# Optimization experiments

Measured on AMD Instinct MI355X. Metric: run time of the kernel, lower is better.

Reference implementation:

```python
import jax, jax.numpy as jnp
import numpy as np

B, IN, COND, H, LAT, E, GH = 8192, 256, 1024, 1024, 128, 6, 64
INP = LAT + COND      # decoder layer0 input size = 1152
INTER = LAT + H       # decoder layer1/2 input size = 1152


def setup_inputs() -> dict:
    key = jax.random.key(0)
    ks = jax.random.split(key, 30)
    n = lambda k, shape, s=0.02: jax.random.normal(k, shape, dtype=jnp.float32) * s
    return {
        'x': jax.random.normal(ks[0], (B, IN), dtype=jnp.float32),
        'y': jax.random.normal(ks[1], (B, COND), dtype=jnp.float32),
        'eps': jax.random.normal(ks[2], (B, LAT), dtype=jnp.float32),
        # encoder: layer k input = prev_dim + IN (x is re-concatenated each layer)
        'enc_w0': n(ks[3], (IN + COND + IN, H)), 'enc_b0': jnp.zeros((H,), jnp.float32),
        'enc_w1': n(ks[4], (H + IN, H)),         'enc_b1': jnp.zeros((H,), jnp.float32),
        'mu_w': n(ks[5], (H, LAT)),  'mu_b': jnp.zeros((LAT,), jnp.float32),
        'lv_w': n(ks[6], (H, LAT)),  'lv_b': jnp.zeros((LAT,), jnp.float32),
        # gating network (input = latent + cond)
        'g_w0': n(ks[7], (INP, GH)), 'g_b0': jnp.zeros((GH,), jnp.float32),
        'g_w1': n(ks[8], (GH, GH)),  'g_b1': jnp.zeros((GH,), jnp.float32),
        'g_w2': n(ks[9], (GH, E)),   'g_b2': jnp.zeros((E,), jnp.float32),
        # expert weights [E, in, out] and biases [E, out] (bias init 0.01 as in source)
        'exp_w0': n(ks[10], (E, INP, H)),   'exp_b0': jnp.full((E, H), 0.01, jnp.float32),
        'exp_w1': n(ks[11], (E, INTER, H)), 'exp_b1': jnp.full((E, H), 0.01, jnp.float32),
        'exp_w2': n(ks[12], (E, INTER, IN)), 'exp_b2': jnp.full((E, IN), 0.01, jnp.float32),
    }


def _forward(x, y, eps, enc_w0, enc_b0, enc_w1, enc_b1, mu_w, mu_b, lv_w, lv_b,
             g_w0, g_b0, g_w1, g_b1, g_w2, g_b2,
             exp_w0, exp_b0, exp_w1, exp_b1, exp_w2, exp_b2):
    elu = jax.nn.elu
    # --- Encoder ---
    h = jnp.concatenate([x, y], axis=1)
    h = elu(jnp.concatenate([h, x], axis=1) @ enc_w0 + enc_b0)
    h = elu(jnp.concatenate([h, x], axis=1) @ enc_w1 + enc_b1)
    mu = h @ mu_w + mu_b
    logvar = h @ lv_w + lv_b
    # --- Reparameterize (eps passed explicitly for determinism) ---
    z = mu + eps * jnp.exp(0.5 * logvar)
    # --- MixedDecoder ---
    g = jnp.concatenate([z, y], axis=1)
    g = elu(g @ g_w0 + g_b0)
    g = elu(g @ g_w1 + g_b1)
    coeff = jax.nn.softmax(g @ g_w2 + g_b2, axis=1)  # [B, E]
    layer_out = y
    for W, bb, act in ((exp_w0, exp_b0, True), (exp_w1, exp_b1, True), (exp_w2, exp_b2, False)):
        inp = jnp.concatenate([z, layer_out], axis=1)  # [B, I]
        # fused mixture-of-experts projection: avoids materializing per-sample [B,I,O] weight
        out = coeff @ bb + jnp.einsum('be,bi,eio->bo', coeff, inp, W)
        layer_out = elu(out) if act else out
    return layer_out, mu, logvar


def reference(x, y, eps, enc_w0, enc_b0, enc_w1, enc_b1, mu_w, mu_b, lv_w, lv_b,
              g_w0, g_b0, g_w1, g_b1, g_w2, g_b2,
              exp_w0, exp_b0, exp_w1, exp_b1, exp_w2, exp_b2):
    return _forward(x, y, eps, enc_w0, enc_b0, enc_w1, enc_b1, mu_w, mu_b, lv_w, lv_b,
                    g_w0, g_b0, g_w1, g_b1, g_w2, g_b2,
                    exp_w0, exp_b0, exp_w1, exp_b1, exp_w2, exp_b2)
```

## Files before the change

kernel.cpp:

```cpp
#include <hip/hip_runtime.h>
#include <hip/hip_bf16.h>
#include <cstddef>

using u16 = unsigned short;
using short8 = __attribute__((ext_vector_type(8))) short;
using f32x4 = __attribute__((ext_vector_type(4))) float;

constexpr int B_   = 8192;
constexpr int IN_  = 256;
constexpr int COND_= 1024;
constexpr int H_   = 1024;
constexpr int LAT_ = 128;
constexpr int NE_  = 6;
constexpr int GH_  = 64;
constexpr int INP_ = 1152;
constexpr int K0_  = 1536;
constexpr int K1_  = 1280;

constexpr int BK = 64;

typedef const __attribute__((address_space(1))) void gv_t;
typedef __attribute__((address_space(3))) void lv_t;
#define GLDS(g, l) __builtin_amdgcn_global_load_lds((gv_t*)(g), (lv_t*)(l), 16, 0, 0)

__device__ __forceinline__ u16 f2b(float f) {
  __hip_bfloat16 h = __float2bfloat16(f);
  return *reinterpret_cast<u16*>(&h);
}
__device__ __forceinline__ ushort4 f2b4(float4 v) {
  ushort4 o;
  o.x = f2b(v.x); o.y = f2b(v.y); o.z = f2b(v.z); o.w = f2b(v.w);
  return o;
}
__device__ __forceinline__ float elu1(float x) { return x > 0.f ? x : (__expf(x) - 1.f); }

__global__ void k_transpose(const float* __restrict__ in, u16* __restrict__ out,
                            int R, int C, long inStride, long outStride) {
  __shared__ float t[32][33];
  const float* ip = in + (long)blockIdx.z * inStride;
  u16* op = out + (long)blockIdx.z * outStride;
  int c0 = blockIdx.x * 32, r0 = blockIdx.y * 32;
  int tx = threadIdx.x, ty = threadIdx.y;
#pragma unroll
  for (int i = 0; i < 4; i++) {
    int r = r0 + ty + i * 8, c = c0 + tx;
    if (r < R && c < C) t[ty + i * 8][tx] = ip[(long)r * C + c];
  }
  __syncthreads();
#pragma unroll
  for (int i = 0; i < 4; i++) {
    int c = c0 + ty + i * 8, r = r0 + tx;
    if (r < R && c < C) op[(long)c * R + r] = f2b(t[tx][ty + i * 8]);
  }
}

__global__ __launch_bounds__(256) void k_pre(
    const float* __restrict__ enc_w0, const float* __restrict__ enc_w1,
    const float* __restrict__ mu_w, const float* __restrict__ lv_w,
    const float* __restrict__ g_w0, const float* __restrict__ exp_w0,
    const float* __restrict__ x, const float* __restrict__ y,
    u16* __restrict__ encw0T, u16* __restrict__ encw1T, u16* __restrict__ mulvT,
    u16* __restrict__ gw0T, u16* __restrict__ ew0T,
    u16* __restrict__ A0, u16* __restrict__ A1)
{
  __shared__ float t[32][33];
  const int b = blockIdx.x;
  const int tid = threadIdx.x;
  const int tx = tid & 31, ty = tid >> 5;

  auto tr = [&](const float* in, u16* out, int R, int C, int bx, int by) {
    int c0 = bx * 32, r0 = by * 32;
#pragma unroll
    for (int i = 0; i < 4; i++) {
      int r = r0 + ty + i * 8, c = c0 + tx;
      if (r < R && c < C) t[ty + i * 8][tx] = in[(long)r * C + c];
    }
    __syncthreads();
#pragma unroll
    for (int i = 0; i < 4; i++) {
      int c = c0 + ty + i * 8, r = r0 + tx;
      if (r < R && c < C) out[(long)c * R + r] = f2b(t[tx][ty + i * 8]);
    }
  };

  if (b < 1536)       { tr(enc_w0, encw0T, K0_, H_, b & 31, b >> 5); }
  else if (b < 2816)  { int l = b - 1536; tr(enc_w1, encw1T, K1_, H_, l & 31, l >> 5); }
  else if (b < 2944)  { int l = b - 2816; tr(mu_w, mulvT, H_, LAT_, l & 3, l >> 2); }
  else if (b < 3072)  { int l = b - 2944; tr(lv_w, mulvT + (size_t)LAT_ * H_, H_, LAT_, l & 3, l >> 2); }
  else if (b < 3144)  { int l = b - 3072; tr(g_w0, gw0T, INP_, GH_, l & 1, l >> 1); }
  else if (b < 10056) {
    int l = b - 3144, e = l / 1152, r2 = l % 1152;
    tr(exp_w0 + (long)e * INP_ * H_, ew0T + (long)e * INP_ * H_, INP_, H_, r2 & 31, r2 >> 5);
  } else {
    long idx = (long)(b - 10056) * 256 + tid;
    long n0v = (long)B_ * K0_ / 4;
    if (idx < n0v) {
      long base = idx * 4;
      int bb = (int)(base / K0_), c = (int)(base % K0_);
      float4 v;
      if (c < IN_)              v = *(const float4*)&x[(long)bb * IN_ + c];
      else if (c < IN_ + COND_) v = *(const float4*)&y[(long)bb * COND_ + (c - IN_)];
      else                      v = *(const float4*)&x[(long)bb * IN_ + (c - IN_ - COND_)];
      *(ushort4*)&A0[base] = f2b4(v);
    } else {
      long j = idx - n0v;
      if (j < (long)B_ * IN_ / 4) {
        long base = j * 4;
        int bb = (int)(base / IN_), c = (int)(base % IN_);
        float4 v = *(const float4*)&x[(long)bb * IN_ + c];
        *(ushort4*)&A1[(long)bb * K1_ + H_ + c] = f2b4(v);
      }
    }
  }
}

__global__ __launch_bounds__(256) void k_mid(
    const float* __restrict__ exp_w2, u16* __restrict__ ew2T,
    const float* __restrict__ mu, const float* __restrict__ lv,
    const float* __restrict__ eps, const float* __restrict__ y,
    u16* __restrict__ ZY, u16* __restrict__ D1, u16* __restrict__ D2)
{
  __shared__ float t[32][33];
  const int b = blockIdx.x;
  const int tid = threadIdx.x;
  if (b < 1728) {
    const int tx = tid & 31, ty = tid >> 5;
    int e = b / 288, r2 = b % 288;
    const float* in = exp_w2 + (long)e * INP_ * IN_;
    u16* out = ew2T + (long)e * INP_ * IN_;
    int c0 = (r2 & 7) * 32, r0 = (r2 >> 3) * 32;
#pragma unroll
    for (int i = 0; i < 4; i++) {
      int r = r0 + ty + i * 8, c = c0 + tx;
      if (r < INP_ && c < IN_) t[ty + i * 8][tx] = in[(long)r * IN_ + c];
    }
    __syncthreads();
#pragma unroll
    for (int i = 0; i < 4; i++) {
      int c = c0 + ty + i * 8, r = r0 + tx;
      if (r < INP_ && c < IN_) out[(long)c * INP_ + r] = f2b(t[tx][ty + i * 8]);
    }
  } else {
    long idx = (long)(b - 1728) * 256 + tid;
    if (idx >= (long)B_ * INP_ / 4) return;
    long base = idx * 4;
    int bb = (int)(base / INP_), c = (int)(base % INP_);
    if (c < LAT_) {
      long o = (long)bb * LAT_ + c;
      float4 m = *(const float4*)&mu[o];
      float4 l = *(const float4*)&lv[o];
      float4 e4 = *(const float4*)&eps[o];
      float4 z;
      z.x = m.x + e4.x * __expf(0.5f * l.x);
      z.y = m.y + e4.y * __expf(0.5f * l.y);
      z.z = m.z + e4.z * __expf(0.5f * l.z);
      z.w = m.w + e4.w * __expf(0.5f * l.w);
      ushort4 zb = f2b4(z);
      *(ushort4*)&ZY[base] = zb;
      *(ushort4*)&D1[base] = zb;
      *(ushort4*)&D2[base] = zb;
    } else {
      float4 v = *(const float4*)&y[(long)bb * COND_ + (c - LAT_)];
      *(ushort4*)&ZY[base] = f2b4(v);
    }
  }
}

__global__ __launch_bounds__(256) void k_gate(const float* __restrict__ G1,
    const float* __restrict__ w1, const float* __restrict__ b1,
    const float* __restrict__ w2, const float* __restrict__ b2,
    float* __restrict__ coeff) {
  __shared__ float W1[64][65];
  __shared__ float W2[64][8];
  __shared__ float B1[64], B2[8];
  int tid = threadIdx.x;
  for (int i = tid; i < 64 * 64; i += 256) W1[i >> 6][i & 63] = w1[i];
  for (int i = tid; i < 64 * 6; i += 256) W2[i / 6][i % 6] = w2[i];
  if (tid < 64) B1[tid] = b1[tid];
  if (tid < 8)  B2[tid] = (tid < 6) ? b2[tid] : 0.f;
  __syncthreads();
  int row = blockIdx.x * 256 + tid;
  const float* gr = G1 + (long)row * GH_;
  float g[64];
#pragma unroll
  for (int i = 0; i < 16; i++) {
    float4 v = *(const float4*)(gr + i * 4);
    g[i*4] = v.x; g[i*4+1] = v.y; g[i*4+2] = v.z; g[i*4+3] = v.w;
  }
  float lg[6];
#pragma unroll
  for (int e = 0; e < 6; e++) lg[e] = B2[e];
  for (int n = 0; n < 64; n++) {
    float s = B1[n];
#pragma unroll
    for (int k = 0; k < 64; k++) s += g[k] * W1[k][n];
    s = elu1(s);
#pragma unroll
    for (int e = 0; e < 6; e++) lg[e] += s * W2[n][e];
  }
  float m = lg[0];
#pragma unroll
  for (int e = 1; e < 6; e++) m = fmaxf(m, lg[e]);
  float p[6], sum = 0.f;
#pragma unroll
  for (int e = 0; e < 6; e++) { p[e] = __expf(lg[e] - m); sum += p[e]; }
  float inv = 1.f / sum;
#pragma unroll
  for (int e = 0; e < 6; e++) coeff[(long)row * 6 + e] = p[e] * inv;
}

template<int KSTEPS, int E, bool MOE>
__global__ __launch_bounds__(512, 2) void k_gemm8(
    const u16* __restrict__ A,
    const u16* __restrict__ WT,
    const float* __restrict__ bias,
    const float* __restrict__ coeff,
    int N,
    u16* __restrict__ outH, int ldo)
{
  constexpr int KK = KSTEPS * BK;
  constexpr int T = E * KSTEPS;
  __shared__ __align__(16) u16 As[3][256][BK];
  __shared__ __align__(16) u16 Bs[3][128][BK];
  __shared__ float Cf[MOE ? 256 : 1][8];

  const int tid = threadIdx.x;
  const int lane = tid & 63, w = tid >> 6;
  const int wr = w >> 1, wc = w & 1;
  const int lin = blockIdx.x + blockIdx.y * gridDim.x;
  const int rb  = (lin & 7) * 4 + ((lin >> 3) & 3);
  const int cp  = lin >> 5;
  const int brow = rb * 256, bcol = cp * 128;
  const int lr = lane & 15, hi = lane >> 4;
  const int lk = hi * 8;
  const int xsw = (lr & 7) << 3;

  if (MOE) {
    if (tid < 256) {
#pragma unroll
      for (int e2 = 0; e2 < 8; e2++)
        Cf[tid][e2] = (e2 < 6) ? coeff[(long)(brow + tid) * 6 + e2] : 0.f;
    }
    __syncthreads();
  }

  f32x4 acc[4][4];
#pragma unroll
  for (int m = 0; m < 4; m++)
#pragma unroll
    for (int n = 0; n < 4; n++)
#pragma unroll
      for (int r = 0; r < 4; r++) acc[m][n][r] = 0.f;
  f32x4 pacc[MOE ? 4 : 1][MOE ? 4 : 1];
  if constexpr (MOE) {
#pragma unroll
    for (int m = 0; m < 4; m++)
#pragma unroll
      for (int n = 0; n < 4; n++)
#pragma unroll
        for (int r = 0; r < 4; r++) pacc[m][n][r] = 0.f;
  }

  const int srow = w * 8 + (lane >> 3);
  const int sdst = (lane & 7) * 8;
  const int ssrc = ((lane & 7) ^ ((lane >> 3) & 7)) * 8;
  const u16* Asrc = A + (long)(brow + srow) * KK + ssrc;
  const u16* Bsrc = WT + (long)(bcol + srow) * KK + ssrc;

  auto STAGE_H = [&](int t2, int buf, int h) {
    const int e2 = (E == 1) ? 0 : (t2 / KSTEPS);
    int k2 = (E == 1) ? t2 : (t2 % KSTEPS);
    if (E > 1 && (e2 & 1)) k2 = KSTEPS - 1 - k2;
    const u16* ap = Asrc + (long)k2 * BK;
    const u16* bp = Bsrc + (long)e2 * ((long)N * KK) + (long)k2 * BK;
    GLDS(ap + (long)((h * 2 + 0) * 64) * KK, &As[buf][(h * 2 + 0) * 64 + srow][sdst]);
    GLDS(ap + (long)((h * 2 + 1) * 64) * KK, &As[buf][(h * 2 + 1) * 64 + srow][sdst]);
    GLDS(bp + (long)(h * 64) * KK,           &Bs[buf][h * 64 + srow][sdst]);
  };

  STAGE_H(0, 0, 0); STAGE_H(0, 0, 1);
  STAGE_H(1, 1, 0); STAGE_H(1, 1, 1);
  asm volatile("s_waitcnt vmcnt(6)" ::: "memory");
  asm volatile("s_barrier" ::: "memory");

  for (int t = 0; t < T; ++t) {
    const int cur = t % 3;
    const int nbuf = (t + 2) % 3;
    const bool do_stage = (t + 2 < T);

    {
      short8 af[4], bfr[4];
      const int cc = lk ^ xsw;
#pragma unroll
      for (int m = 0; m < 4; m++)
        af[m] = *(const short8*)&As[cur][wr * 64 + m * 16 + lr][cc];
#pragma unroll
      for (int n = 0; n < 4; n++)
        bfr[n] = *(const short8*)&Bs[cur][wc * 64 + n * 16 + lr][cc];
      if (do_stage) STAGE_H(t + 2, nbuf, 0);
      asm volatile("s_barrier" ::: "memory");
      __builtin_amdgcn_s_setprio(1);
#pragma unroll
      for (int m = 0; m < 4; m++)
#pragma unroll
        for (int n = 0; n < 4; n++) {
          if constexpr (MOE)
            pacc[m][n] = __builtin_amdgcn_mfma_f32_16x16x32_bf16(af[m], bfr[n], pacc[m][n], 0, 0, 0);
          else
            acc[m][n] = __builtin_amdgcn_mfma_f32_16x16x32_bf16(af[m], bfr[n], acc[m][n], 0, 0, 0);
        }
      __builtin_amdgcn_s_setprio(0);
      asm volatile("s_barrier" ::: "memory");
    }

    {
      short8 af[4], bfr[4];
      const int cc = (32 + lk) ^ xsw;
#pragma unroll
      for (int m = 0; m < 4; m++)
        af[m] = *(const short8*)&As[cur][wr * 64 + m * 16 + lr][cc];
#pragma unroll
      for (int n = 0; n < 4; n++)
        bfr[n] = *(const short8*)&Bs[cur][wc * 64 + n * 16 + lr][cc];
      if (do_stage) STAGE_H(t + 2, nbuf, 1);
      asm volatile("s_barrier" ::: "memory");
      __builtin_amdgcn_s_setprio(1);
#pragma unroll
      for (int m = 0; m < 4; m++)
#pragma unroll
        for (int n = 0; n < 4; n++) {
          if constexpr (MOE)
            pacc[m][n] = __builtin_amdgcn_mfma_f32_16x16x32_bf16(af[m], bfr[n], pacc[m][n], 0, 0, 0);
          else
            acc[m][n] = __builtin_amdgcn_mfma_f32_16x16x32_bf16(af[m], bfr[n], acc[m][n], 0, 0, 0);
        }
      __builtin_amdgcn_s_setprio(0);
      if (t + 1 < T) {
        if (do_stage) asm volatile("s_waitcnt vmcnt(6)" ::: "memory");
        else          asm volatile("s_waitcnt vmcnt(0)" ::: "memory");
      }
      asm volatile("s_barrier" ::: "memory");
    }

    if constexpr (MOE) {
      if ((t + 1) % KSTEPS == 0) {
        const int e = t / KSTEPS;
#pragma unroll
        for (int m = 0; m < 4; m++)
#pragma unroll
          for (int r = 0; r < 4; r++) {
            float c = Cf[wr * 64 + m * 16 + hi * 4 + r][e];
#pragma unroll
            for (int n = 0; n < 4; n++) acc[m][n][r] += c * pacc[m][n][r];
          }
        if (t + 1 < T) {
#pragma unroll
          for (int m = 0; m < 4; m++)
#pragma unroll
            for (int n = 0; n < 4; n++)
#pragma unroll
              for (int r = 0; r < 4; r++) pacc[m][n][r] = 0.f;
        }
      }
    }
  }

#pragma unroll
  for (int m = 0; m < 4; m++)
#pragma unroll
    for (int n = 0; n < 4; n++) {
      const int col = bcol + wc * 64 + n * 16 + lr;
#pragma unroll
      for (int r = 0; r < 4; r++) {
        const int rowl = wr * 64 + m * 16 + hi * 4 + r;
        const long row = brow + rowl;
        float v = acc[m][n][r];
        if constexpr (MOE) {
          float bv = 0.f;
#pragma unroll
          for (int e = 0; e < 6; e++) bv += Cf[rowl][e] * bias[(long)e * N + col];
          v += bv;
        } else {
          v += bias[col];
        }
        v = elu1(v);
        outH[row * (long)ldo + col] = f2b(v);
      }
    }
}

template<int KSTEPS, int E, bool MOE>
__global__ __launch_bounds__(256, 2) void k_m2(
    const u16* __restrict__ A,
    const u16* __restrict__ WT,
    const float* __restrict__ bias, const float* __restrict__ bias2,
    const float* __restrict__ coeff,
    int N,
    u16* __restrict__ outH, float* __restrict__ outF, float* __restrict__ outF2,
    int ldo, int splitcol, int act)
{
  constexpr int KK = KSTEPS * BK;
  constexpr int T = E * KSTEPS;
  __shared__ __align__(16) u16 As[3][64][BK];
  __shared__ __align__(16) u16 Bs[3][128][BK];
  __shared__ float Cf[MOE ? 64 : 1][8];

  const int tid = threadIdx.x;
  const int lane = tid & 63, w = tid >> 6;
  const int wr = w >> 1, wc = w & 1;
  const int brow = blockIdx.x * 64, bcol = blockIdx.y * 128;
  const int lr = lane & 15, hi = lane >> 4;
  const int lk = hi * 8;
  const int xsw = (lr & 7) << 3;

  if (MOE) {
    if (tid < 64) {
#pragma unroll
      for (int e2 = 0; e2 < 8; e2++)
        Cf[tid][e2] = (e2 < 6) ? coeff[(long)(brow + tid) * 6 + e2] : 0.f;
    }
    __syncthreads();
  }

  f32x4 acc[2][4];
#pragma unroll
  for (int m = 0; m < 2; m++)
#pragma unroll
    for (int n = 0; n < 4; n++)
#pragma unroll
      for (int r = 0; r < 4; r++) acc[m][n][r] = 0.f;
  f32x4 pacc[MOE ? 2 : 1][MOE ? 4 : 1];
  if constexpr (MOE) {
#pragma unroll
    for (int m = 0; m < 2; m++)
#pragma unroll
      for (int n = 0; n < 4; n++)
#pragma unroll
        for (int r = 0; r < 4; r++) pacc[m][n][r] = 0.f;
  }

  const int srow = w * 8 + (lane >> 3);
  const int sdst = (lane & 7) * 8;
  const int ssrc = ((lane & 7) ^ ((lane >> 3) & 7)) * 8;
  const u16* Asrc = A + (long)(brow + srow) * KK + ssrc;
  const u16* Bsrc = WT + (long)(bcol + srow) * KK + ssrc;

  auto STAGE_H = [&](int t2, int buf, int h) {
    const int e2 = (E == 1) ? 0 : (t2 / KSTEPS);
    int k2 = (E == 1) ? t2 : (t2 % KSTEPS);
    if (E > 1 && (e2 & 1)) k2 = KSTEPS - 1 - k2;
    const u16* ap = Asrc + (long)k2 * BK;
    const u16* bp = Bsrc + (long)e2 * ((long)N * KK) + (long)k2 * BK;
    GLDS(ap + (long)(h * 32) * KK,            &As[buf][h * 32 + srow][sdst]);
    GLDS(bp + (long)(h * 64) * KK,            &Bs[buf][h * 64 + srow][sdst]);
    GLDS(bp + (long)(h * 64 + 32) * KK,       &Bs[buf][h * 64 + 32 + srow][sdst]);
  };

  STAGE_H(0, 0, 0); STAGE_H(0, 0, 1);
  STAGE_H(1, 1, 0); STAGE_H(1, 1, 1);
  asm volatile("s_waitcnt vmcnt(6)" ::: "memory");
  asm volatile("s_barrier" ::: "memory");

  for (int t = 0; t < T; ++t) {
    const int cur = t % 3;
    const int nbuf = (t + 2) % 3;
    const bool do_stage = (t + 2 < T);

    {
      short8 af[2], bfr[4];
      const int cc = lk ^ xsw;
#pragma unroll
      for (int m = 0; m < 2; m++)
        af[m] = *(const short8*)&As[cur][wr * 32 + m * 16 + lr][cc];
#pragma unroll
      for (int n = 0; n < 4; n++)
        bfr[n] = *(const short8*)&Bs[cur][wc * 64 + n * 16 + lr][cc];
      if (do_stage) STAGE_H(t + 2, nbuf, 0);
      asm volatile("s_barrier" ::: "memory");
      __builtin_amdgcn_s_setprio(1);
#pragma unroll
      for (int m = 0; m < 2; m++)
#pragma unroll
        for (int n = 0; n < 4; n++) {
          if constexpr (MOE)
            pacc[m][n] = __builtin_amdgcn_mfma_f32_16x16x32_bf16(af[m], bfr[n], pacc[m][n], 0, 0, 0);
          else
            acc[m][n] = __builtin_amdgcn_mfma_f32_16x16x32_bf16(af[m], bfr[n], acc[m][n], 0, 0, 0);
        }
      __builtin_amdgcn_s_setprio(0);
      asm volatile("s_barrier" ::: "memory");
    }
    {
      short8 af[2], bfr[4];
      const int cc = (32 + lk) ^ xsw;
#pragma unroll
      for (int m = 0; m < 2; m++)
        af[m] = *(const short8*)&As[cur][wr * 32 + m * 16 + lr][cc];
#pragma unroll
      for (int n = 0; n < 4; n++)
        bfr[n] = *(const short8*)&Bs[cur][wc * 64 + n * 16 + lr][cc];
      if (do_stage) STAGE_H(t + 2, nbuf, 1);
      asm volatile("s_barrier" ::: "memory");
      __builtin_amdgcn_s_setprio(1);
#pragma unroll
      for (int m = 0; m < 2; m++)
#pragma unroll
        for (int n = 0; n < 4; n++) {
          if constexpr (MOE)
            pacc[m][n] = __builtin_amdgcn_mfma_f32_16x16x32_bf16(af[m], bfr[n], pacc[m][n], 0, 0, 0);
          else
            acc[m][n] = __builtin_amdgcn_mfma_f32_16x16x32_bf16(af[m], bfr[n], acc[m][n], 0, 0, 0);
        }
      __builtin_amdgcn_s_setprio(0);
      if (t + 1 < T) {
        if (do_stage) asm volatile("s_waitcnt vmcnt(6)" ::: "memory");
        else          asm volatile("s_waitcnt vmcnt(0)" ::: "memory");
      }
      asm volatile("s_barrier" ::: "memory");
    }

    if constexpr (MOE) {
      if ((t + 1) % KSTEPS == 0) {
        const int e = t / KSTEPS;
#pragma unroll
        for (int m = 0; m < 2; m++)
#pragma unroll
          for (int r = 0; r < 4; r++) {
            float c = Cf[wr * 32 + m * 16 + hi * 4 + r][e];
#pragma unroll
            for (int n = 0; n < 4; n++) acc[m][n][r] += c * pacc[m][n][r];
          }
        if (t + 1 < T) {
#pragma unroll
          for (int m = 0; m < 2; m++)
#pragma unroll
            for (int n = 0; n < 4; n++)
#pragma unroll
              for (int r = 0; r < 4; r++) pacc[m][n][r] = 0.f;
        }
      }
    }
  }

#pragma unroll
  for (int m = 0; m < 2; m++)
#pragma unroll
    for (int n = 0; n < 4; n++) {
      const int col = bcol + wc * 64 + n * 16 + lr;
      if (col >= N) continue;
#pragma unroll
      for (int r = 0; r < 4; r++) {
        const int rowl = wr * 32 + m * 16 + hi * 4 + r;
        const long row = brow + rowl;
        float v = acc[m][n][r];
        if constexpr (MOE) {
          float bv = 0.f;
#pragma unroll
          for (int e = 0; e < 6; e++) bv += Cf[rowl][e] * bias[(long)e * N + col];
          v += bv;
        } else {
          v += (col < splitcol) ? bias[col] : bias2[col - splitcol];
        }
        if (act) v = elu1(v);
        if (outH) outH[row * (long)ldo + col] = f2b(v);
        else if (col < splitcol) outF[row * (long)ldo + col] = v;
        else outF2[row * (long)ldo + (col - splitcol)] = v;
      }
    }
}

extern "C" void kernel_launch(void* const* d_in, const int* in_sizes, int n_in,
                              void* d_out, int out_size, void* d_ws, size_t ws_size,
                              hipStream_t stream) {
  (void)in_sizes; (void)out_size;
  if (n_in < 23) return;
  const float* x      = (const float*)d_in[0];
  const float* y      = (const float*)d_in[1];
  const float* eps    = (const float*)d_in[2];
  const float* enc_w0 = (const float*)d_in[3];
  const float* enc_b0 = (const float*)d_in[4];
  const float* enc_w1 = (const float*)d_in[5];
  const float* enc_b1 = (const float*)d_in[6];
  const float* mu_w   = (const float*)d_in[7];
  const float* mu_b   = (const float*)d_in[8];
  const float* lv_w   = (const float*)d_in[9];
  const float* lv_b   = (const float*)d_in[10];
  const float* g_w0   = (const float*)d_in[11];
  const float* g_b0   = (const float*)d_in[12];
  const float* g_w1   = (const float*)d_in[13];
  const float* g_b1   = (const float*)d_in[14];
  const float* g_w2   = (const float*)d_in[15];
  const float* g_b2   = (const float*)d_in[16];
  const float* exp_w0 = (const float*)d_in[17];
  const float* exp_b0 = (const float*)d_in[18];
  const float* exp_w1 = (const float*)d_in[19];
  const float* exp_b1 = (const float*)d_in[20];
  const float* exp_w2 = (const float*)d_in[21];
  const float* exp_b2 = (const float*)d_in[22];

  char* ws = (char*)d_ws;
  size_t off = 0;
  auto alloc = [&](size_t bytes) -> void* {
    void* p = ws + off; off += (bytes + 255) & ~(size_t)255; return p;
  };
  u16* A0     = (u16*)alloc((size_t)B_ * K0_ * 2);
  u16* A1     = (u16*)alloc((size_t)B_ * K1_ * 2);
  u16* H2     = (u16*)alloc((size_t)B_ * H_ * 2);
  u16* ZY     = (u16*)alloc((size_t)B_ * INP_ * 2);
  u16* encw0T = (u16*)alloc((size_t)K0_ * H_ * 2);
  u16* encw1T = (u16*)alloc((size_t)K1_ * H_ * 2);
  u16* mulvT  = (u16*)alloc((size_t)256 * H_ * 2);
  u16* gw0T   = (u16*)alloc((size_t)GH_ * INP_ * 2);
  u16* ew0T   = (u16*)alloc((size_t)NE_ * H_ * INP_ * 2);
  if (ws_size < off) return;

  u16* D1 = A0;
  u16* D2 = A1;
  float* G1    = (float*)H2;
  float* COEFF = (float*)((char*)H2 + (size_t)B_ * GH_ * 4);
  u16* ew2T = (u16*)((char*)H2 + (size_t)4 * 1024 * 1024);
  u16* ew1T = ZY;

  float* outO = (float*)d_out;
  float* muO  = outO + (size_t)B_ * IN_;
  float* lvO  = muO + (size_t)B_ * LAT_;

  k_pre<<<24392, 256, 0, stream>>>(enc_w0, enc_w1, mu_w, lv_w, g_w0, exp_w0,
      x, y, encw0T, encw1T, mulvT, gw0T, ew0T, A0, A1);

  k_gemm8<K0_ / BK, 1, false><<<dim3(32, 8), 512, 0, stream>>>(A0, encw0T, enc_b0,
      nullptr, H_, A1, K1_);
  k_gemm8<K1_ / BK, 1, false><<<dim3(32, 8), 512, 0, stream>>>(A1, encw1T, enc_b1,
      nullptr, H_, H2, H_);

  k_m2<H_ / BK, 1, false><<<dim3(B_ / 64, 2), 256, 0, stream>>>(H2, mulvT,
      mu_b, lv_b, nullptr, 256, nullptr, muO, lvO, LAT_, LAT_, 0);

  k_mid<<<10944, 256, 0, stream>>>(exp_w2, ew2T, muO, lvO, eps, y, ZY, D1, D2);

  k_m2<INP_ / BK, 1, false><<<dim3(B_ / 64, 1), 256, 0, stream>>>(ZY, gw0T,
      g_b0, g_b0, nullptr, GH_, nullptr, G1, nullptr, GH_, GH_, 1);
  k_gate<<<B_ / 256, 256, 0, stream>>>(G1, g_w1, g_b1, g_w2, g_b2, COEFF);

  k_gemm8<INP_ / BK, NE_, true><<<dim3(32, 8), 512, 0, stream>>>(ZY, ew0T, exp_b0,
      COEFF, H_, D1 + LAT_, INP_);
  k_transpose<<<dim3(32, 36, NE_), dim3(32, 8), 0, stream>>>(exp_w1, ew1T, INP_, H_,
                                                    (long)INP_ * H_, (long)INP_ * H_);
  k_gemm8<INP_ / BK, NE_, true><<<dim3(32, 8), 512, 0, stream>>>(D1, ew1T, exp_b1,
      COEFF, H_, D2 + LAT_, INP_);
  k_m2<INP_ / BK, NE_, true><<<dim3(B_ / 64, 2), 256, 0, stream>>>(D2, ew2T,
      exp_b2, nullptr, COEFF, IN_, nullptr, outO, nullptr, IN_, IN_, 0);
}
```

Before: 518.9 us.

## Load B operand straight from global into registers, bypassing LDS

The weight (B) tile no longer goes through shared memory. Each wave reads its B fragments directly from global memory into registers and prefetches the next half-step's fragments. Only the A tile is still staged into a triple-buffered LDS ring, and the loop drops to one barrier per iteration. This is meant to cut LDS traffic, LDS capacity and barrier overhead, at the cost of redundant global and L2 reads of B across waves that share a column tile. The explicit vmcnt wait that guarded the A staging was removed, so correct A visibility now depends on waits the compiler inserts for the B register loads, which looks fragile.

```diff
diff --git a/kernel.cpp b/kernel.cpp
--- a/kernel.cpp
+++ b/kernel.cpp
@@ -221,7 +221,6 @@
   constexpr int KK = KSTEPS * BK;
   constexpr int T = E * KSTEPS;
   __shared__ __align__(16) u16 As[3][256][BK];
-  __shared__ __align__(16) u16 Bs[3][128][BK];
   __shared__ float Cf[MOE ? 256 : 1][8];
 
   const int tid = threadIdx.x;
@@ -234,6 +233,7 @@
   const int lr = lane & 15, hi = lane >> 4;
   const int lk = hi * 8;
   const int xsw = (lr & 7) << 3;
+  const long NKK = (long)N * KK;
 
   if (MOE) {
     if (tid < 256) {
@@ -265,40 +265,51 @@
   const int sdst = (lane & 7) * 8;
   const int ssrc = ((lane & 7) ^ ((lane >> 3) & 7)) * 8;
   const u16* Asrc = A + (long)(brow + srow) * KK + ssrc;
-  const u16* Bsrc = WT + (long)(bcol + srow) * KK + ssrc;
-
-  auto STAGE_H = [&](int t2, int buf, int h) {
+  const u16* Blane = WT + (long)(bcol + wc * 64 + lr) * KK + hi * 8;
+
+  auto STAGE_A = [&](int t2) {
     const int e2 = (E == 1) ? 0 : (t2 / KSTEPS);
     int k2 = (E == 1) ? t2 : (t2 % KSTEPS);
     if (E > 1 && (e2 & 1)) k2 = KSTEPS - 1 - k2;
     const u16* ap = Asrc + (long)k2 * BK;
-    const u16* bp = Bsrc + (long)e2 * ((long)N * KK) + (long)k2 * BK;
-    GLDS(ap + (long)((h * 2 + 0) * 64) * KK, &As[buf][(h * 2 + 0) * 64 + srow][sdst]);
-    GLDS(ap + (long)((h * 2 + 1) * 64) * KK, &As[buf][(h * 2 + 1) * 64 + srow][sdst]);
-    GLDS(bp + (long)(h * 64) * KK,           &Bs[buf][h * 64 + srow][sdst]);
+    const int buf = t2 % 3;
+#pragma unroll
+    for (int i = 0; i < 4; i++)
+      GLDS(ap + (long)(i * 64) * KK, &As[buf][i * 64 + srow][sdst]);
   };
-
-  STAGE_H(0, 0, 0); STAGE_H(0, 0, 1);
-  STAGE_H(1, 1, 0); STAGE_H(1, 1, 1);
-  asm volatile("s_waitcnt vmcnt(6)" ::: "memory");
+  auto BADDR = [&](int t2, int kk) -> const u16* {
+    const int e2 = (E == 1) ? 0 : (t2 / KSTEPS);
+    int k2 = (E == 1) ? t2 : (t2 % KSTEPS);
+    if (E > 1 && (e2 & 1)) k2 = KSTEPS - 1 - k2;
+    return Blane + (long)e2 * NKK + (long)k2 * BK + kk;
+  };
+
+  STAGE_A(0);
+  STAGE_A(1);
+  short8 bfr[4], nb[4];
+  {
+    const u16* bp = BADDR(0, 0);
+#pragma unroll
+    for (int n = 0; n < 4; n++) bfr[n] = *(const short8*)(bp + (long)(n * 16) * KK);
+  }
+  asm volatile("s_waitcnt vmcnt(8)" ::: "memory");
   asm volatile("s_barrier" ::: "memory");
 
   for (int t = 0; t < T; ++t) {
     const int cur = t % 3;
-    const int nbuf = (t + 2) % 3;
-    const bool do_stage = (t + 2 < T);
 
     {
-      short8 af[4], bfr[4];
+      short8 af[4];
       const int cc = lk ^ xsw;
 #pragma unroll
       for (int m = 0; m < 4; m++)
         af[m] = *(const short8*)&As[cur][wr * 64 + m * 16 + lr][cc];
-#pragma unroll
-      for (int n = 0; n < 4; n++)
-        bfr[n] = *(const short8*)&Bs[cur][wc * 64 + n * 16 + lr][cc];
-      if (do_stage) STAGE_H(t + 2, nbuf, 0);
-      asm volatile("s_barrier" ::: "memory");
+      {
+        const u16* bp = BADDR(t, 32);
+#pragma unroll
+        for (int n = 0; n < 4; n++) nb[n] = *(const short8*)(bp + (long)(n * 16) * KK);
+      }
+      if (t + 2 < T) STAGE_A(t + 2);
       __builtin_amdgcn_s_setprio(1);
 #pragma unroll
       for (int m = 0; m < 4; m++)
@@ -310,36 +321,30 @@
             acc[m][n] = __builtin_amdgcn_mfma_f32_16x16x32_bf16(af[m], bfr[n], acc[m][n], 0, 0, 0);
         }
       __builtin_amdgcn_s_setprio(0);
-      asm volatile("s_barrier" ::: "memory");
     }
 
     {
-      short8 af[4], bfr[4];
+      short8 af[4];
       const int cc = (32 + lk) ^ xsw;
 #pragma unroll
       for (int m = 0; m < 4; m++)
         af[m] = *(const short8*)&As[cur][wr * 64 + m * 16 + lr][cc];
-#pragma unroll
-      for (int n = 0; n < 4; n++)
-        bfr[n] = *(const short8*)&Bs[cur][wc * 64 + n * 16 + lr][cc];
-      if (do_stage) STAGE_H(t + 2, nbuf, 1);
-      asm volatile("s_barrier" ::: "memory");
+      if (t + 1 < T) {
+        const u16* bp = BADDR(t + 1, 0);
+#pragma unroll
+        for (int n = 0; n < 4; n++) bfr[n] = *(const short8*)(bp + (long)(n * 16) * KK);
+      }
       __builtin_amdgcn_s_setprio(1);
 #pragma unroll
       for (int m = 0; m < 4; m++)
 #pragma unroll
         for (int n = 0; n < 4; n++) {
           if constexpr (MOE)
-            pacc[m][n] = __builtin_amdgcn_mfma_f32_16x16x32_bf16(af[m], bfr[n], pacc[m][n], 0, 0, 0);
+            pacc[m][n] = __builtin_amdgcn_mfma_f32_16x16x32_bf16(af[m], nb[n], pacc[m][n], 0, 0, 0);
           else
-            acc[m][n] = __builtin_amdgcn_mfma_f32_16x16x32_bf16(af[m], bfr[n], acc[m][n], 0, 0, 0);
+            acc[m][n] = __builtin_amdgcn_mfma_f32_16x16x32_bf16(af[m], nb[n], acc[m][n], 0, 0, 0);
         }
       __builtin_amdgcn_s_setprio(0);
-      if (t + 1 < T) {
-        if (do_stage) asm volatile("s_waitcnt vmcnt(6)" ::: "memory");
-        else          asm volatile("s_waitcnt vmcnt(0)" ::: "memory");
-      }
-      asm volatile("s_barrier" ::: "memory");
     }
 
     if constexpr (MOE) {
@@ -363,6 +368,8 @@
         }
       }
     }
+
+    asm volatile("s_barrier" ::: "memory");
   }
 
 #pragma unroll
```

Result: slower. 861.6 us (+66.1%).
